# Kernel optimization log

Measured on AMD Instinct MI355X. Metric: run time of the kernel, lower is better.

## Reference

```python
import jax, jax.numpy as jnp
import numpy as np
import math

B, QL, KL, D = 8, 2048, 2048, 1024


def setup_inputs() -> dict:
    key = jax.random.key(0)
    ks = jax.random.split(key, 9)
    s = 1.0 / math.sqrt(D)
    return {
        "q_embd": jax.random.normal(ks[0], (B, QL, D), jnp.float32),
        "k_embd": jax.random.normal(ks[1], (B, KL, D), jnp.float32),
        "v_embd": jax.random.normal(ks[2], (B, KL, D), jnp.float32),
        "Wq": jax.random.normal(ks[3], (D, D), jnp.float32) * s,
        "bq": jax.random.normal(ks[4], (D,), jnp.float32) * s,
        "Wk": jax.random.normal(ks[5], (D, D), jnp.float32) * s,
        "bk": jax.random.normal(ks[6], (D,), jnp.float32) * s,
        "Wv": jax.random.normal(ks[7], (D, D), jnp.float32) * s,
        "bv": jax.random.normal(ks[8], (D,), jnp.float32) * s,
    }


def reference(q_embd, k_embd, v_embd, Wq, bq, Wk, bk, Wv, bv):
    # Linear projections (torch Linear: x @ W^T + b); head_size==1 so
    # the permute/view multi-head reshuffle is an identity.
    q = jnp.einsum("bsd,hd->bsh", q_embd, Wq) + bq  # [B,QL,D]
    k = jnp.einsum("bsd,hd->bsh", k_embd, Wk) + bk  # [B,KL,D]
    v = jnp.einsum("bsd,hd->bsh", v_embd, Wv) + bv  # [B,KL,D]
    # scaled_dot score: [B,QL,KL]
    scale = 1.0 / jnp.sqrt(jnp.asarray(q.shape[-1], q.dtype))
    score = jnp.einsum("bqd,bkd->bqk", q, k) * scale
    attn = jax.nn.softmax(score, axis=-1)
    out = jnp.einsum("bqk,bkd->bqd", attn, v)  # [B,QL,D]
    return out
```

## Files before the change

kernel.cpp:

```cpp
#include <hip/hip_runtime.h>
#include <hip/hip_bf16.h>

typedef float f32x4 __attribute__((ext_vector_type(4)));
typedef __bf16 bf16x8 __attribute__((ext_vector_type(8)));
typedef unsigned short u16x4 __attribute__((ext_vector_type(4)));

__device__ __forceinline__ unsigned short f2bf(float f) {
  unsigned u = __builtin_bit_cast(unsigned, f);
  u += 0x7FFFu + ((u >> 16) & 1u);
  return (unsigned short)(u >> 16);
}
__device__ __forceinline__ float bf2f(unsigned short h) {
  unsigned u = ((unsigned)h) << 16;
  return __builtin_bit_cast(float, u);
}

__device__ __forceinline__ void gload_lds16(const void* g, void* l) {
  __builtin_amdgcn_global_load_lds(
      (const __attribute__((address_space(1))) void*)g,
      (__attribute__((address_space(3))) void*)l, 16, 0, 0);
}

constexpr int BM = 256, BN = 256, BK = 64;

#define BAR() __builtin_amdgcn_s_barrier()
#define VMW(N) asm volatile("s_waitcnt vmcnt(" #N ")" ::: "memory")
#define PRIO(x) __builtin_amdgcn_s_setprio(x)

#define MM(a_, b_, c_)                                                        \
  c_ = __builtin_amdgcn_mfma_f32_16x16x32_bf16(                               \
      __builtin_bit_cast(bf16x8, a_), __builtin_bit_cast(bf16x8, b_), c_, 0, 0, 0)

template <int OUT_MODE, bool HAS_BIAS, int FMODE>
__global__ __launch_bounds__(512, 2) void gemm256(
    const unsigned short* __restrict__ A, const unsigned short* __restrict__ B,
    const float* __restrict__ bias, float scale, void* __restrict__ Cv,
    int N, int K, long sA, long sB, long sC, float* __restrict__ rsum,
    int gx, int gy) {
  __shared__ char sm[131072];

  const int nwg = gridDim.x;
  int id = blockIdx.x;
  id = (id & 7) * (nwg >> 3) + (id >> 3);
  const int bx = id % gx;
  const int by = (id / gx) % gy;
  const int bz = id / (gx * gy);

  const int t = threadIdx.x;
  const int lane = t & 63;
  const int w = t >> 6;
  const int wm = w >> 2;
  const int wn = w & 3;

  const int rowBase = by * BM;
  const int colBase = bx * BN;
  const unsigned short* Ab = A + sA * bz;
  const unsigned short* Bb = B + sB * bz;
  const int NT = K >> 6;

  const int srl = lane >> 3;
  const int schunk = (lane & 7) ^ srl;

#define STAGE_A(tt, h, d)                                                     \
  do {                                                                        \
    int _kt = (tt); if (_kt > NT - 1) _kt = NT - 1;                           \
    const int _k0 = _kt << 6;                                                 \
    _Pragma("unroll") for (int _j = 0; _j < 2; ++_j) {                        \
      const int _r = (w + 8 * _j) * 8 + srl;                                  \
      gload_lds16(Ab + (size_t)(rowBase + (h) * 128 + _r) * K + _k0 + schunk * 8, \
                  sm + (d) * 32768 + (h) * 16384 + (w + 8 * _j) * 1024);      \
    }                                                                         \
  } while (0)
#define STAGE_B(tt, h, d)                                                     \
  do {                                                                        \
    int _kt = (tt); if (_kt > NT - 1) _kt = NT - 1;                           \
    const int _k0 = _kt << 6;                                                 \
    _Pragma("unroll") for (int _j = 0; _j < 2; ++_j) {                        \
      const int _r = (w + 8 * _j) * 8 + srl;                                  \
      gload_lds16(Bb + (size_t)(colBase + (h) * 128 + _r) * K + _k0 + schunk * 8, \
                  sm + 65536 + (d) * 32768 + (h) * 16384 + (w + 8 * _j) * 1024); \
    }                                                                         \
  } while (0)

  const int lr = lane & 15;
  const int g0 = lane >> 4;
  const int sw0 = (g0 ^ (lr & 7)) << 4;
  const int sw1 = ((g0 + 4) ^ (lr & 7)) << 4;
  const int aBase = wm * 8192 + lr * 128;
  const int bBase = 65536 + wn * 4096 + lr * 128;

  uint4 Ar[4][2], Br0[2][2], Br1[2][2];
  f32x4 acc[8][4];
#pragma unroll
  for (int m = 0; m < 8; ++m)
#pragma unroll
    for (int n = 0; n < 4; ++n) acc[m][n] = (f32x4){0.f, 0.f, 0.f, 0.f};

#define READ_A(d, mh)                                                         \
  do {                                                                        \
    _Pragma("unroll") for (int f = 0; f < 4; ++f) {                           \
      Ar[f][0] = *(const uint4*)(sm + (d) * 32768 + (mh) * 16384 + aBase + f * 2048 + sw0); \
      Ar[f][1] = *(const uint4*)(sm + (d) * 32768 + (mh) * 16384 + aBase + f * 2048 + sw1); \
    }                                                                         \
  } while (0)
#define READ_B0(d)                                                            \
  do {                                                                        \
    _Pragma("unroll") for (int f = 0; f < 2; ++f) {                           \
      Br0[f][0] = *(const uint4*)(sm + (d) * 32768 + bBase + f * 2048 + sw0); \
      Br0[f][1] = *(const uint4*)(sm + (d) * 32768 + bBase + f * 2048 + sw1); \
    }                                                                         \
  } while (0)
#define READ_B1(d)                                                            \
  do {                                                                        \
    _Pragma("unroll") for (int f = 0; f < 2; ++f) {                           \
      Br1[f][0] = *(const uint4*)(sm + (d) * 32768 + 16384 + bBase + f * 2048 + sw0); \
      Br1[f][1] = *(const uint4*)(sm + (d) * 32768 + 16384 + bBase + f * 2048 + sw1); \
    }                                                                         \
  } while (0)

#define MFMA_Q(Bset, mh, nh)                                                  \
  do {                                                                        \
    _Pragma("unroll") for (int kk = 0; kk < 2; ++kk)                          \
        _Pragma("unroll") for (int mf = 0; mf < 4; ++mf)                      \
            _Pragma("unroll") for (int nf = 0; nf < 2; ++nf)                  \
                MM(Ar[mf][kk], Bset[nf][kk], acc[(mh) * 4 + mf][(nh) * 2 + nf]); \
  } while (0)

#define TILE2(t_, d_)                                                         \
  do {                                                                        \
     READ_B0(d_); READ_B1(d_); READ_A(d_, 0);                       \
    STAGE_A((t_) + 1, 1, (d_) ^ 1);                                           \
    BAR();                                                                    \
    PRIO(1); MFMA_Q(Br0, 0, 0); MFMA_Q(Br1, 0, 1); PRIO(0);                   \
    BAR();                                                                    \
     READ_A(d_, 1);                                                 \
    STAGE_A((t_) + 2, 0, d_); STAGE_B((t_) + 2, 0, d_); STAGE_B((t_) + 2, 1, d_); \
    BAR();                                                                    \
    PRIO(1); MFMA_Q(Br1, 1, 1); MFMA_Q(Br0, 1, 0); PRIO(0);                   \
    VMW(6);                                                                   \
    BAR();                                                                    \
  } while (0)

  STAGE_A(0, 0, 0); STAGE_B(0, 0, 0); STAGE_B(0, 1, 0); STAGE_A(0, 1, 0);
  STAGE_A(1, 0, 1); STAGE_B(1, 0, 1); STAGE_B(1, 1, 1);
  VMW(6);
  BAR();

  for (int i = 0; i < (NT >> 1); ++i) {
    TILE2(2 * i, 0);
    TILE2(2 * i + 1, 1);
  }
  VMW(0);

  if constexpr (OUT_MODE == 3 && FMODE > 0) {
    unsigned short* C = (unsigned short*)Cv + sC * bz;
    float* smf = (float*)sm;
    if constexpr (FMODE == 1) __syncthreads();
#pragma unroll
    for (int m = 0; m < 8; ++m) {
      const int row0 = rowBase + (m >> 2) * 128 + wm * 64 + (m & 3) * 16 + g0 * 4;
      f32x4 rs = (f32x4){0.f, 0.f, 0.f, 0.f};
#pragma unroll
      for (int n = 0; n < 4; ++n) {
        const int col = colBase + (n >> 1) * 128 + wn * 32 + (n & 1) * 16 + lr;
        f32x4 v = acc[m][n];
#pragma unroll
        for (int r = 0; r < 4; ++r) {
          const unsigned short h = f2bf(__expf(v[r] * scale));
          C[(size_t)(row0 + r) * N + col] = h;
          rs[r] += bf2f(h);
        }
      }
#pragma unroll
      for (int mk = 1; mk < 16; mk <<= 1) {
        rs[0] += __shfl_xor(rs[0], mk);
        rs[1] += __shfl_xor(rs[1], mk);
        rs[2] += __shfl_xor(rs[2], mk);
        rs[3] += __shfl_xor(rs[3], mk);
      }
      if (lr == 0) {
        if constexpr (FMODE == 2) {
#pragma unroll
          for (int r = 0; r < 4; ++r)
            rsum[((size_t)bz * 2048 + row0 + r) * 32 + bx * 4 + wn] = rs[r];
        } else {
          const int lrow = row0 - rowBase;
#pragma unroll
          for (int r = 0; r < 4; ++r) smf[wn * 256 + lrow + r] = rs[r];
        }
      }
    }
    if constexpr (FMODE == 1) {
      __syncthreads();
      if (t < 256) {
        const float s4 = smf[t] + smf[256 + t] + smf[512 + t] + smf[768 + t];
        rsum[((size_t)bz * 2048 + rowBase + t) * 8 + bx] = s4;
      }
    }
  } else if constexpr (OUT_MODE == 3) {
    unsigned short* C = (unsigned short*)Cv + sC * bz;
#pragma unroll
    for (int n = 0; n < 4; ++n) {
      const int col = colBase + (n >> 1) * 128 + wn * 32 + (n & 1) * 16 + lr;
#pragma unroll
      for (int m = 0; m < 8; ++m) {
        const int row0 = rowBase + (m >> 2) * 128 + wm * 64 + (m & 3) * 16 + g0 * 4;
        f32x4 v = acc[m][n];
#pragma unroll
        for (int r = 0; r < 4; ++r)
          C[(size_t)(row0 + r) * N + col] = f2bf(__expf(v[r] * scale));
      }
    }
  } else if constexpr (OUT_MODE == 2) {
    float* C = (float*)Cv + sC * bz;
    float* smf = (float*)sm;
    if constexpr (FMODE == 2) {
      __syncthreads();
      if (t < 256) {
        const size_t pb = ((size_t)bz * 2048 + rowBase + t) * 32;
        float s = 0.f;
#pragma unroll
        for (int q = 0; q < 8; ++q) {
          const float4 p = *(const float4*)&rsum[pb + q * 4];
          s += ((p.x + p.y) + (p.z + p.w));
        }
        smf[t] = 1.f / s;
      }
      __syncthreads();
    }
#pragma unroll
    for (int m = 0; m < 8; ++m) {
      const int row0 = rowBase + (m >> 2) * 128 + wm * 64 + (m & 3) * 16 + g0 * 4;
      f32x4 inv;
      if constexpr (FMODE == 2) {
        const int lrow = row0 - rowBase;
#pragma unroll
        for (int r = 0; r < 4; ++r) inv[r] = smf[lrow + r];
      } else if constexpr (FMODE == 1) {
#pragma unroll
        for (int r = 0; r < 4; ++r) {
          const size_t pb = ((size_t)bz * 2048 + row0 + r) * 8;
          const float4 p0 = *(const float4*)&rsum[pb];
          const float4 p1 = *(const float4*)&rsum[pb + 4];
          inv[r] = 1.f / (((p0.x + p0.y) + (p0.z + p0.w)) +
                          ((p1.x + p1.y) + (p1.z + p1.w)));
        }
      } else {
        const float4 lv = *(const float4*)&rsum[(size_t)bz * 2048 + row0];
        inv[0] = 1.f / lv.x; inv[1] = 1.f / lv.y;
        inv[2] = 1.f / lv.z; inv[3] = 1.f / lv.w;
      }
#pragma unroll
      for (int n = 0; n < 4; ++n) {
        const int col = colBase + (n >> 1) * 128 + wn * 32 + (n & 1) * 16 + lr;
        f32x4 v = acc[m][n];
#pragma unroll
        for (int r = 0; r < 4; ++r)
          C[(size_t)(row0 + r) * N + col] = v[r] * inv[r];
      }
    }
  } else {
#pragma unroll
    for (int n = 0; n < 4; ++n) {
      const int col = colBase + (n >> 1) * 128 + wn * 32 + (n & 1) * 16 + lr;
      float bvv = 0.f;
      if constexpr (HAS_BIAS) bvv = bias[col];
#pragma unroll
      for (int m = 0; m < 8; ++m) {
        const int row0 = rowBase + (m >> 2) * 128 + wm * 64 + (m & 3) * 16 + g0 * 4;
        f32x4 v = acc[m][n];
        if constexpr (OUT_MODE == 0) {
          unsigned short* C = (unsigned short*)Cv + sC * bz;
#pragma unroll
          for (int r = 0; r < 4; ++r)
            C[(size_t)(row0 + r) * N + col] = f2bf(v[r] * scale + bvv);
        } else {
          unsigned short* C = (unsigned short*)Cv;
          const int b = row0 >> 11, s = row0 & 2047;
          u16x4 pk;
#pragma unroll
          for (int r = 0; r < 4; ++r) pk[r] = f2bf(v[r] * scale + bvv);
          *(u16x4*)&C[((size_t)b * N + col) * 2048 + s] = pk;
        }
      }
    }
  }
}

__global__ __launch_bounds__(256) void conv_pair(
    const float* __restrict__ e, const float* __restrict__ wt,
    unsigned short* __restrict__ eo, unsigned short* __restrict__ wo,
    int ne8, int nw8) {
  const int tot = ne8 + nw8;
  const int stride = gridDim.x * 256;
  for (int i = blockIdx.x * 256 + threadIdx.x; i < tot; i += stride) {
    const float* src;
    unsigned short* dst;
    int k;
    if (i < ne8) { src = e; dst = eo; k = i; }
    else { src = wt; dst = wo; k = i - ne8; }
    float4 a = ((const float4*)src)[2 * k];
    float4 b = ((const float4*)src)[2 * k + 1];
    unsigned short h[8];
    h[0] = f2bf(a.x); h[1] = f2bf(a.y); h[2] = f2bf(a.z); h[3] = f2bf(a.w);
    h[4] = f2bf(b.x); h[5] = f2bf(b.y); h[6] = f2bf(b.z); h[7] = f2bf(b.w);
    ((uint4*)dst)[k] = *(uint4*)h;
  }
}

__global__ __launch_bounds__(256) void rowsum_kernel(
    const unsigned short* __restrict__ E, float* __restrict__ out) {
  const size_t row = blockIdx.x;
  const unsigned short* p = E + row * 2048;
  const int t = threadIdx.x;
  const int lane = t & 63, wid = t >> 6;

  uint4 x = ((const uint4*)p)[t];
  const unsigned short* hs = (const unsigned short*)&x;
  float s = 0.f;
#pragma unroll
  for (int j = 0; j < 8; ++j) s += bf2f(hs[j]);
#pragma unroll
  for (int d = 1; d < 64; d <<= 1) s += __shfl_xor(s, d);
  __shared__ float red[4];
  if (lane == 0) red[wid] = s;
  __syncthreads();
  if (t == 0) out[row] = red[0] + red[1] + red[2] + red[3];
}

extern "C" void kernel_launch(void* const* d_in, const int* in_sizes, int n_in,
                              void* d_out, int out_size, void* d_ws, size_t ws_size,
                              hipStream_t stream) {
  const float* q_embd = (const float*)d_in[0];
  const float* k_embd = (const float*)d_in[1];
  const float* v_embd = (const float*)d_in[2];
  const float* Wq = (const float*)d_in[3];
  const float* bq = (const float*)d_in[4];
  const float* Wk = (const float*)d_in[5];
  const float* bk = (const float*)d_in[6];
  const float* Wv = (const float*)d_in[7];
  const float* bv = (const float*)d_in[8];

  constexpr int B = 8, QL = 2048, KL = 2048, D = 1024;
  constexpr size_t NE = (size_t)B * QL * D;
  constexpr size_t LAYOUT_BYTES = 3 * NE * 2 + (size_t)B * QL * KL * 2;
  constexpr size_t P8_BYTES = (size_t)B * QL * 8 * 4;
  constexpr size_t P32_BYTES = (size_t)B * QL * 32 * 4;

  unsigned short* qb = (unsigned short*)d_ws;
  unsigned short* kb = qb + NE;
  unsigned short* vT = kb + NE;
  unsigned short* Sb = vT + NE;
  unsigned short* Xe = Sb;
  unsigned short* Wb = Sb + NE;

  const int fmode = ws_size >= LAYOUT_BYTES + P32_BYTES ? 2
                  : ws_size >= LAYOUT_BYTES + P8_BYTES  ? 1 : 0;
  float* partial = fmode ? (float*)((char*)d_ws + LAYOUT_BYTES) : (float*)qb;

  dim3 blk256(256), blk512(512);
  const dim3 gconv(2048);
  const dim3 gproj(4 * 64);
  constexpr int NE8 = (int)(NE / 8), NW8 = D * D / 8;

  conv_pair<<<gconv, blk256, 0, stream>>>(q_embd, Wq, Xe, Wb, NE8, NW8);
  gemm256<0, true, 0><<<gproj, blk512, 0, stream>>>(
      Xe, Wb, bq, 1.0f, qb, D, D, 0L, 0L, 0L, nullptr, 4, 64);
  conv_pair<<<gconv, blk256, 0, stream>>>(k_embd, Wk, Xe, Wb, NE8, NW8);
  gemm256<0, true, 0><<<gproj, blk512, 0, stream>>>(
      Xe, Wb, bk, 1.0f, kb, D, D, 0L, 0L, 0L, nullptr, 4, 64);
  conv_pair<<<gconv, blk256, 0, stream>>>(v_embd, Wv, Xe, Wb, NE8, NW8);
  gemm256<1, true, 0><<<gproj, blk512, 0, stream>>>(
      Xe, Wb, bv, 1.0f, vT, D, D, 0L, 0L, 0L, nullptr, 4, 64);

  if (fmode == 2) {
    gemm256<3, false, 2><<<dim3(512), blk512, 0, stream>>>(
        qb, kb, nullptr, 0.03125f, Sb, KL, D, (long)QL * D, (long)KL * D,
        (long)QL * KL, partial, 8, 8);
  } else if (fmode == 1) {
    gemm256<3, false, 1><<<dim3(512), blk512, 0, stream>>>(
        qb, kb, nullptr, 0.03125f, Sb, KL, D, (long)QL * D, (long)KL * D,
        (long)QL * KL, partial, 8, 8);
  } else {
    gemm256<3, false, 0><<<dim3(512), blk512, 0, stream>>>(
        qb, kb, nullptr, 0.03125f, Sb, KL, D, (long)QL * D, (long)KL * D,
        (long)QL * KL, nullptr, 8, 8);
    rowsum_kernel<<<dim3(B * QL), blk256, 0, stream>>>(Sb, partial);
  }

  if (fmode == 2) {
    gemm256<2, false, 2><<<dim3(256), blk512, 0, stream>>>(
        Sb, vT, nullptr, 1.0f, d_out, D, KL, (long)QL * KL, (long)D * KL,
        (long)QL * D, partial, 4, 8);
  } else if (fmode == 1) {
    gemm256<2, false, 1><<<dim3(256), blk512, 0, stream>>>(
        Sb, vT, nullptr, 1.0f, d_out, D, KL, (long)QL * KL, (long)D * KL,
        (long)QL * D, partial, 4, 8);
  } else {
    gemm256<2, false, 0><<<dim3(256), blk512, 0, stream>>>(
        Sb, vT, nullptr, 1.0f, d_out, D, KL, (long)QL * KL, (long)D * KL,
        (long)QL * D, partial, 4, 8);
  }
}
```

Before: 343.2 us.

## Fuse fp32-to-bf16 activation conversion into projection GEMM A-operand loads

Removes the three separate passes that converted each fp32 embedding tensor to bf16 before its projection GEMM. A new GEMM variant loads fp32 A tiles into registers, converts them to bf16 and writes them into swizzled LDS one tile ahead, while B (weights) is still staged via the existing path. All three weight matrices are converted once in a single small kernel. This saves a full fp32 read plus bf16 write/read of each activation tensor, but adds register pressure (occupancy lowered to 1 block per CU) and conversion ALU work inside the GEMM main loop.

Result: no change. 344.3 us (+0.3%).

```diff
diff --git a/kernel.cpp b/kernel.cpp
--- a/kernel.cpp
+++ b/kernel.cpp
@@ -24,6 +24,11 @@
 constexpr int BM = 256, BN = 256, BK = 64;
 
 #define BAR() __builtin_amdgcn_s_barrier()
+#define LGKM0()                                        \
+  do {                                                 \
+    asm volatile("s_waitcnt lgkmcnt(0)" ::: "memory"); \
+    __builtin_amdgcn_sched_barrier(0);                 \
+  } while (0)
 #define VMW(N) asm volatile("s_waitcnt vmcnt(" #N ")" ::: "memory")
 #define PRIO(x) __builtin_amdgcn_s_setprio(x)
 
@@ -287,18 +292,149 @@
   }
 }
 
-__global__ __launch_bounds__(256) void conv_pair(
-    const float* __restrict__ e, const float* __restrict__ wt,
-    unsigned short* __restrict__ eo, unsigned short* __restrict__ wo,
-    int ne8, int nw8) {
-  const int tot = ne8 + nw8;
+template <int OUT_MODE>
+__global__ __launch_bounds__(512, 1) void gemmP(
+    const float* __restrict__ Ap, const unsigned short* __restrict__ Bw,
+    const float* __restrict__ bias, void* __restrict__ Cv, int N, int K,
+    int gx, int gy) {
+  __shared__ char sm[131072];
+
+  const int nwg = gridDim.x;
+  int id = blockIdx.x;
+  id = (id & 7) * (nwg >> 3) + (id >> 3);
+  const int bx = id % gx;
+  const int by = (id / gx) % gy;
+
+  const int t = threadIdx.x;
+  const int lane = t & 63;
+  const int w = t >> 6;
+  const int wm = w >> 2;
+  const int wn = w & 3;
+
+  const int rowBase = by * BM;
+  const int colBase = bx * BN;
+  const unsigned short* Bb = Bw;
+  const int NT = K >> 6;
+
+  const int srl = lane >> 3;
+  const int schunk = (lane & 7) ^ srl;
+
+  const int ar = t >> 2;
+  const int as0 = (t & 3) * 2;
+
+  const int lr = lane & 15;
+  const int g0 = lane >> 4;
+  const int sw0 = (g0 ^ (lr & 7)) << 4;
+  const int sw1 = ((g0 + 4) ^ (lr & 7)) << 4;
+  const int aBase = wm * 8192 + lr * 128;
+  const int bBase = 65536 + wn * 4096 + lr * 128;
+
+  uint4 Ar[4][2], Br0[2][2], Br1[2][2];
+  float4 Areg[2][4];
+  f32x4 acc[8][4];
+#pragma unroll
+  for (int m = 0; m < 8; ++m)
+#pragma unroll
+    for (int n = 0; n < 4; ++n) acc[m][n] = (f32x4){0.f, 0.f, 0.f, 0.f};
+
+#define LOAD_AP(tt)                                                           \
+  do {                                                                        \
+    int _kt = (tt); if (_kt > NT - 1) _kt = NT - 1;                           \
+    _Pragma("unroll") for (int _h = 0; _h < 2; ++_h) {                        \
+      const float* _ap = Ap + (size_t)(rowBase + _h * 128 + ar) * K +         \
+                         (_kt << 6) + as0 * 8;                                \
+      _Pragma("unroll") for (int _j = 0; _j < 2; ++_j) {                      \
+        Areg[_h][_j * 2 + 0] = *(const float4*)(_ap + _j * 8);                \
+        Areg[_h][_j * 2 + 1] = *(const float4*)(_ap + _j * 8 + 4);            \
+      }                                                                       \
+    }                                                                         \
+  } while (0)
+
+#define CVTW_AP(d)                                                            \
+  do {                                                                        \
+    _Pragma("unroll") for (int _h = 0; _h < 2; ++_h)                          \
+      _Pragma("unroll") for (int _j = 0; _j < 2; ++_j) {                      \
+        unsigned short _hh[8];                                                \
+        const float4 _a = Areg[_h][_j * 2 + 0];                               \
+        const float4 _b = Areg[_h][_j * 2 + 1];                               \
+        _hh[0] = f2bf(_a.x); _hh[1] = f2bf(_a.y);                             \
+        _hh[2] = f2bf(_a.z); _hh[3] = f2bf(_a.w);                             \
+        _hh[4] = f2bf(_b.x); _hh[5] = f2bf(_b.y);                             \
+        _hh[6] = f2bf(_b.z); _hh[7] = f2bf(_b.w);                             \
+        const int _slot = as0 + _j;                                           \
+        *(uint4*)(sm + (d) * 32768 + _h * 16384 + ar * 128 +                  \
+                  ((_slot ^ (ar & 7)) << 4)) = *(uint4*)&_hh[0];              \
+      }                                                                       \
+  } while (0)
+
+#define TILE_P(t_, d_)                                                        \
+  do {                                                                        \
+    READ_B0(d_); READ_B1(d_); READ_A(d_, 0);                                  \
+    CVTW_AP((d_) ^ 1);                                                        \
+    LOAD_AP((t_) + 2);                                                        \
+    LGKM0();                                                                  \
+    BAR();                                                                    \
+    PRIO(1); MFMA_Q(Br0, 0, 0); MFMA_Q(Br1, 0, 1); PRIO(0);                   \
+    BAR();                                                                    \
+    READ_A(d_, 1);                                                            \
+    STAGE_B((t_) + 2, 0, d_); STAGE_B((t_) + 2, 1, d_);                       \
+    BAR();                                                                    \
+    PRIO(1); MFMA_Q(Br1, 1, 1); MFMA_Q(Br0, 1, 0); PRIO(0);                   \
+    VMW(12);                                                                  \
+    BAR();                                                                    \
+  } while (0)
+
+  STAGE_B(0, 0, 0); STAGE_B(0, 1, 0);
+  STAGE_B(1, 0, 1); STAGE_B(1, 1, 1);
+  LOAD_AP(0);
+  CVTW_AP(0);
+  LOAD_AP(1);
+  VMW(0);
+  LGKM0();
+  BAR();
+
+  for (int i = 0; i < NT; ++i) TILE_P(i, i & 1);
+  VMW(0);
+
+#pragma unroll
+  for (int n = 0; n < 4; ++n) {
+    const int col = colBase + (n >> 1) * 128 + wn * 32 + (n & 1) * 16 + lr;
+    const float bvv = bias[col];
+#pragma unroll
+    for (int m = 0; m < 8; ++m) {
+      const int row0 = rowBase + (m >> 2) * 128 + wm * 64 + (m & 3) * 16 + g0 * 4;
+      f32x4 v = acc[m][n];
+      if constexpr (OUT_MODE == 0) {
+        unsigned short* C = (unsigned short*)Cv;
+#pragma unroll
+        for (int r = 0; r < 4; ++r)
+          C[(size_t)(row0 + r) * N + col] = f2bf(v[r] + bvv);
+      } else {
+        unsigned short* C = (unsigned short*)Cv;
+        const int b = row0 >> 11, s = row0 & 2047;
+        u16x4 pk;
+#pragma unroll
+        for (int r = 0; r < 4; ++r) pk[r] = f2bf(v[r] + bvv);
+        *(u16x4*)&C[((size_t)b * N + col) * 2048 + s] = pk;
+      }
+    }
+  }
+}
+
+__global__ __launch_bounds__(256) void conv_w3(
+    const float* __restrict__ w0, const float* __restrict__ w1,
+    const float* __restrict__ w2, unsigned short* __restrict__ o0,
+    unsigned short* __restrict__ o1, unsigned short* __restrict__ o2,
+    int n8each) {
+  const int tot = 3 * n8each;
   const int stride = gridDim.x * 256;
   for (int i = blockIdx.x * 256 + threadIdx.x; i < tot; i += stride) {
     const float* src;
     unsigned short* dst;
     int k;
-    if (i < ne8) { src = e; dst = eo; k = i; }
-    else { src = wt; dst = wo; k = i - ne8; }
+    if (i < n8each) { src = w0; dst = o0; k = i; }
+    else if (i < 2 * n8each) { src = w1; dst = o1; k = i - n8each; }
+    else { src = w2; dst = o2; k = i - 2 * n8each; }
     float4 a = ((const float4*)src)[2 * k];
     float4 b = ((const float4*)src)[2 * k + 1];
     unsigned short h[8];
@@ -343,6 +479,7 @@
 
   constexpr int B = 8, QL = 2048, KL = 2048, D = 1024;
   constexpr size_t NE = (size_t)B * QL * D;
+  constexpr size_t DD = (size_t)D * D;
   constexpr size_t LAYOUT_BYTES = 3 * NE * 2 + (size_t)B * QL * KL * 2;
   constexpr size_t P8_BYTES = (size_t)B * QL * 8 * 4;
   constexpr size_t P32_BYTES = (size_t)B * QL * 32 * 4;
@@ -351,27 +488,23 @@
   unsigned short* kb = qb + NE;
   unsigned short* vT = kb + NE;
   unsigned short* Sb = vT + NE;
-  unsigned short* Xe = Sb;
-  unsigned short* Wb = Sb + NE;
+  unsigned short* Wqb = Sb;
+  unsigned short* Wkb = Sb + DD;
+  unsigned short* Wvb = Sb + 2 * DD;
 
   const int fmode = ws_size >= LAYOUT_BYTES + P32_BYTES ? 2
                   : ws_size >= LAYOUT_BYTES + P8_BYTES  ? 1 : 0;
   float* partial = fmode ? (float*)((char*)d_ws + LAYOUT_BYTES) : (float*)qb;
 
   dim3 blk256(256), blk512(512);
-  const dim3 gconv(2048);
   const dim3 gproj(4 * 64);
-  constexpr int NE8 = (int)(NE / 8), NW8 = D * D / 8;
-
-  conv_pair<<<gconv, blk256, 0, stream>>>(q_embd, Wq, Xe, Wb, NE8, NW8);
-  gemm256<0, true, 0><<<gproj, blk512, 0, stream>>>(
-      Xe, Wb, bq, 1.0f, qb, D, D, 0L, 0L, 0L, nullptr, 4, 64);
-  conv_pair<<<gconv, blk256, 0, stream>>>(k_embd, Wk, Xe, Wb, NE8, NW8);
-  gemm256<0, true, 0><<<gproj, blk512, 0, stream>>>(
-      Xe, Wb, bk, 1.0f, kb, D, D, 0L, 0L, 0L, nullptr, 4, 64);
-  conv_pair<<<gconv, blk256, 0, stream>>>(v_embd, Wv, Xe, Wb, NE8, NW8);
-  gemm256<1, true, 0><<<gproj, blk512, 0, stream>>>(
-      Xe, Wb, bv, 1.0f, vT, D, D, 0L, 0L, 0L, nullptr, 4, 64);
+  constexpr int NW8 = (int)(DD / 8);
+
+  conv_w3<<<dim3(512), blk256, 0, stream>>>(Wq, Wk, Wv, Wqb, Wkb, Wvb, NW8);
+
+  gemmP<0><<<gproj, blk512, 0, stream>>>(q_embd, Wqb, bq, qb, D, D, 4, 64);
+  gemmP<0><<<gproj, blk512, 0, stream>>>(k_embd, Wkb, bk, kb, D, D, 4, 64);
+  gemmP<1><<<gproj, blk512, 0, stream>>>(v_embd, Wvb, bv, vT, D, D, 4, 64);
 
   if (fmode == 2) {
     gemm256<3, false, 2><<<dim3(512), blk512, 0, stream>>>(
```
